# Performance work log

Measured on AMD Instinct MI355X. Metric: run time of the kernel, lower is better.

## Reference

```python
import jax, jax.numpy as jnp
import numpy as np

EPS = 1e-7
MAX_TANGENT_NORM = 1.5
SCALE = 16.0 / 8.0  # alpha / rank


def _exp_map_zero(vs, K, max_norm):
    # vs: [..., n] spatial tangent at origin (time component is 0).
    # Returns (x0, xs): Lorentz point time/spatial parts, <x,x>_L = -1/K.
    sqrtK = jnp.sqrt(K)
    n = jnp.linalg.norm(vs, axis=-1, keepdims=True)
    nc = jnp.minimum(n, max_norm)                       # clamp tangent norm (TB-PAG)
    vs_c = vs * (nc / jnp.maximum(n, EPS))
    t = sqrtK * nc
    x0 = jnp.cosh(t) / sqrtK
    xs = jnp.sinh(t) / (sqrtK * jnp.maximum(nc, EPS)) * vs_c
    return x0, xs


def _log_map_zero_spatial(x0, xs, K):
    # Inverse of exp at origin; returns spatial part of tangent vector.
    sqrtK = jnp.sqrt(K)
    d = jnp.arccosh(jnp.maximum(sqrtK * x0, 1.0 + EPS)) / sqrtK  # geodesic distance
    ns = jnp.linalg.norm(xs, axis=-1, keepdims=True)
    return d * xs / jnp.maximum(ns, EPS)


def setup_inputs() -> dict:
    key = jax.random.key(0)
    k1, k2, k3, k4, k5 = jax.random.split(key, 5)
    Bsz, S, D, R = 4, 2048, 4096, 8
    x = jax.random.normal(k1, (Bsz, S, D), dtype=jnp.float32)
    W = jax.random.normal(k2, (D, D), dtype=jnp.float32) * (1.0 / np.sqrt(D))
    b = jax.random.normal(k3, (D,), dtype=jnp.float32) * 0.01
    A = jax.random.normal(k4, (D, R), dtype=jnp.float32) * 0.01
    B = jax.random.normal(k5, (R, D), dtype=jnp.float32) * 0.01
    log_K = jnp.zeros((), dtype=jnp.float32)  # K = 1.0
    return {"x": x, "W": W, "b": b, "A": A, "B": B, "log_K": log_K}


def reference(x, W, b, A, B, log_K):
    K = jnp.clip(jnp.exp(log_K), 1e-4, 10.0)
    # frozen Euclidean base: z = x @ W^T + b
    z_base = jnp.einsum('bsd,od->bso', x, W) + b
    # project Euclidean hidden state onto H^n: exp_map_zero([0, x])
    x0, xs = _exp_map_zero(x, K, MAX_TANGENT_NORM)
    # LLR: tangent vector at origin, rank-r bottleneck, back to manifold
    v = _log_map_zero_spatial(x0, xs, K)            # [b,s,d]
    v_adapted = (v @ A) @ B                          # rank-8 bottleneck
    y0, ys = _exp_map_zero(v_adapted, K, MAX_TANGENT_NORM)
    # project back to Euclidean (spatial slice of log map)
    delta = _log_map_zero_spatial(y0, ys, K)
    return z_base + delta * SCALE
```

## Files before the change

### kernel.cpp

```cpp
#include <hip/hip_runtime.h>
#include <hip/hip_bf16.h>


#define DD 4096
#define MR 8192
#define BM 256
#define BN 256
#define BK 64

typedef float f32x4 __attribute__((ext_vector_type(4)));
typedef __bf16 bf16x8 __attribute__((ext_vector_type(8)));

#define GLOAD_LDS16(gptr, lptr)                                                        \
  __builtin_amdgcn_global_load_lds((const __attribute__((address_space(1))) void*)(gptr), \
                                   (__attribute__((address_space(3))) void*)(lptr), 16, 0, 0)

__device__ __forceinline__ __bf16 f2bf(float f) { return (__bf16)f; }

__global__ __launch_bounds__(256) void k_prep(const float* __restrict__ x,
                                              const float* __restrict__ W,
                                              const float* __restrict__ A,
                                              const float* __restrict__ Bm,
                                              __bf16* __restrict__ Xb,
                                              __bf16* __restrict__ Wb,
                                              float* __restrict__ U,
                                              float* __restrict__ G) {
  int bid = blockIdx.x;
  int t = threadIdx.x;
  int lane = t & 63, wid = t >> 6;

  if (bid == 0) {
    float g[64];
#pragma unroll
    for (int i = 0; i < 64; ++i) g[i] = 0.f;
    for (int d = t; d < DD; d += 256) {
      float br[8];
#pragma unroll
      for (int r = 0; r < 8; ++r) br[r] = Bm[r * DD + d];
#pragma unroll
      for (int r = 0; r < 8; ++r)
#pragma unroll
        for (int s = 0; s < 8; ++s) g[r * 8 + s] += br[r] * br[s];
    }
    __shared__ float gs[4][64];
#pragma unroll
    for (int i = 0; i < 64; ++i) {
      float v = g[i];
      for (int off = 32; off >= 1; off >>= 1) v += __shfl_down(v, off, 64);
      if (lane == 0) gs[wid][i] = v;
    }
    __syncthreads();
    if (t < 64) G[t] = gs[0][t] + gs[1][t] + gs[2][t] + gs[3][t];
  } else if (bid <= 2048) {
    int r0 = (bid - 1) * 4;
    const float* xr0 = x + (size_t)r0 * DD;
    __bf16* xb0 = Xb + (size_t)r0 * DD;
    float nsq[4] = {0.f, 0.f, 0.f, 0.f};
    float p[4][8] = {};
#pragma unroll
    for (int i = 0; i < 16; ++i) {
      int d = t + 256 * i;
      f32x4 a0 = *reinterpret_cast<const f32x4*>(A + (size_t)d * 8);
      f32x4 a1 = *reinterpret_cast<const f32x4*>(A + (size_t)d * 8 + 4);
#pragma unroll
      for (int r = 0; r < 4; ++r) {
        float xv = xr0[(size_t)r * DD + d];
        xb0[(size_t)r * DD + d] = f2bf(xv);
        nsq[r] += xv * xv;
        p[r][0] += xv * a0[0]; p[r][1] += xv * a0[1];
        p[r][2] += xv * a0[2]; p[r][3] += xv * a0[3];
        p[r][4] += xv * a1[0]; p[r][5] += xv * a1[1];
        p[r][6] += xv * a1[2]; p[r][7] += xv * a1[3];
      }
    }
    for (int off = 32; off >= 1; off >>= 1) {
#pragma unroll
      for (int r = 0; r < 4; ++r) {
        nsq[r] += __shfl_down(nsq[r], off, 64);
#pragma unroll
        for (int q = 0; q < 8; ++q) p[r][q] += __shfl_down(p[r][q], off, 64);
      }
    }
    __shared__ float red[4][36];
    if (lane == 0) {
#pragma unroll
      for (int r = 0; r < 4; ++r) {
        red[wid][r * 9] = nsq[r];
#pragma unroll
        for (int q = 0; q < 8; ++q) red[wid][r * 9 + 1 + q] = p[r][q];
      }
    }
    __syncthreads();
    if (t < 4) {
      float ns = red[0][t * 9] + red[1][t * 9] + red[2][t * 9] + red[3][t * 9];
      float u[8];
#pragma unroll
      for (int q = 0; q < 8; ++q)
        u[q] = red[0][t * 9 + 1 + q] + red[1][t * 9 + 1 + q] +
               red[2][t * 9 + 1 + q] + red[3][t * 9 + 1 + q];
      float n = sqrtf(ns);
      float s1 = fminf(n, 1.5f) / fmaxf(n, 1e-7f);
#pragma unroll
      for (int q = 0; q < 8; ++q) U[(size_t)(r0 + t) * 8 + q] = s1 * u[q];
    }
  } else {
    int i = (bid - 2049) * 256 + t;
    const f32x4* s = reinterpret_cast<const f32x4*>(W) + (size_t)i * 2;
    f32x4 v0 = s[0], v1 = s[1];
    bf16x8 o;
    o[0] = f2bf(v0[0]); o[1] = f2bf(v0[1]); o[2] = f2bf(v0[2]); o[3] = f2bf(v0[3]);
    o[4] = f2bf(v1[0]); o[5] = f2bf(v1[1]); o[6] = f2bf(v1[2]); o[7] = f2bf(v1[3]);
    reinterpret_cast<bf16x8*>(Wb)[i] = o;
  }
}

__global__ __launch_bounds__(512, 2) void k_gemm(const __bf16* __restrict__ Xb,
                                                 const __bf16* __restrict__ Wb,
                                                 const float* __restrict__ bias,
                                                 const float* __restrict__ U,
                                                 const float* __restrict__ G,
                                                 const float* __restrict__ Bm,
                                                 float* __restrict__ out) {
  __shared__ union {
    char raw[131072];
    struct { float cs[256][8]; float bs2[8][256]; } epi;
  } sm;
  char* smc = sm.raw;

  const int nwg = (MR / BM) * (DD / BN);
  int wg = ((int)blockIdx.x % 8) * (nwg / 8) + (int)blockIdx.x / 8;
  int tm = wg / (DD / BN);
  int tn = wg % (DD / BN);
  int row0 = tm * BM, col0 = tn * BN;

  int t = threadIdx.x;
  int lane = t & 63, wid = t >> 6;
  int wm = wid >> 2, wn = wid & 3;
  int fr = lane & 15;
  int hi = lane >> 4;
  int sw = (fr >> 1) & 3;

  f32x4 acc[8][4] = {};
  bf16x8 aF[4], bF[4];

  auto STAGE = [&](const __bf16* mat, int rowbase, int tau, int ks, int ldsOff) {
    int j = (t & 3) ^ ((t >> 3) & 3);
    int kk = ((tau & 63) << 6) + (ks << 5) + (j << 3);
    const __bf16* src = mat + (size_t)(rowbase + (t >> 2)) * DD + kk;
    char* dst = smc + ldsOff + t * 16;
    GLOAD_LDS16(src, dst);
    GLOAD_LDS16(src + (size_t)128 * DD, dst + 8192);
  };

#define LDA(buf, ks, mbase)                                                     \
  _Pragma("unroll") for (int j = 0; j < 4; ++j) aF[j] =                         \
      *reinterpret_cast<const bf16x8*>(smc + (buf)*65536 + 16384 + (ks)*32768 + \
                                       (wm * 128 + ((mbase) + j) * 16 + fr) * 64 + \
                                       ((hi ^ sw) << 4));
#define LDB(buf, ks)                                                            \
  _Pragma("unroll") for (int j = 0; j < 4; ++j) bF[j] =                         \
      *reinterpret_cast<const bf16x8*>(smc + (buf)*65536 + (ks)*32768 +         \
                                       (wn * 64 + j * 16 + fr) * 64 +           \
                                       ((hi ^ sw) << 4));
#define MMQ(mbase)                                                              \
  __builtin_amdgcn_s_setprio(1);                                                \
  _Pragma("unroll") for (int j = 0; j < 4; ++j)                                 \
      _Pragma("unroll") for (int n = 0; n < 4; ++n)                             \
          acc[(mbase) + j][n] = __builtin_amdgcn_mfma_f32_16x16x32_bf16(        \
              aF[j], bF[n], acc[(mbase) + j][n], 0, 0, 0);                      \
  __builtin_amdgcn_s_setprio(0);
#define BAR() __builtin_amdgcn_s_barrier()
#define VM6() asm volatile("s_waitcnt vmcnt(6)" ::: "memory")

  STAGE(Wb, col0, 0, 0, 0);
  STAGE(Xb, row0, 0, 0, 16384);
  STAGE(Wb, col0, 0, 1, 32768);
  STAGE(Xb, row0, 0, 1, 49152);
  asm volatile("s_waitcnt vmcnt(4)" ::: "memory");
  STAGE(Wb, col0, 1, 0, 65536 + 0);
  STAGE(Xb, row0, 1, 0, 65536 + 16384);
  STAGE(Wb, col0, 1, 1, 65536 + 32768);
  VM6();
  BAR();

  for (int i = 0; i < 32; ++i) {
    int T = 2 * i;
    LDA(0, 0, 0); LDB(0, 0);
    STAGE(Xb, row0, T + 1, 1, 65536 + 49152);
    BAR();
    MMQ(0);
    BAR();
    LDA(0, 0, 4);
    STAGE(Wb, col0, T + 2, 0, 0);
    BAR();
    MMQ(4);
    BAR();
    LDA(0, 1, 0); LDB(0, 1);
    STAGE(Xb, row0, T + 2, 0, 16384);
    BAR();
    MMQ(0);
    BAR();
    LDA(0, 1, 4);
    STAGE(Wb, col0, T + 2, 1, 32768);
    BAR();
    MMQ(4);
    VM6();
    BAR();
    LDA(1, 0, 0); LDB(1, 0);
    STAGE(Xb, row0, T + 2, 1, 49152);
    BAR();
    MMQ(0);
    BAR();
    LDA(1, 0, 4);
    STAGE(Wb, col0, T + 3, 0, 65536 + 0);
    BAR();
    MMQ(4);
    BAR();
    LDA(1, 1, 0); LDB(1, 1);
    STAGE(Xb, row0, T + 3, 0, 65536 + 16384);
    BAR();
    MMQ(0);
    BAR();
    LDA(1, 1, 4);
    STAGE(Wb, col0, T + 3, 1, 65536 + 32768);
    BAR();
    MMQ(4);
    VM6();
    BAR();
  }

  asm volatile("s_waitcnt vmcnt(0)" ::: "memory");
  __syncthreads();
  {
    int rr = t >> 6, cc = (t & 63) * 4;
    *reinterpret_cast<f32x4*>(&sm.epi.bs2[rr][cc]) =
        *reinterpret_cast<const f32x4*>(Bm + (size_t)rr * DD + col0 + cc);
  }
  if (t < 256) {
    f32x4 u0 = *reinterpret_cast<const f32x4*>(U + (size_t)(row0 + t) * 8);
    f32x4 u1 = *reinterpret_cast<const f32x4*>(U + (size_t)(row0 + t) * 8 + 4);
    float u[8] = {u0[0], u0[1], u0[2], u0[3], u1[0], u1[1], u1[2], u1[3]};
    float n2sq = 0.f;
#pragma unroll
    for (int r = 0; r < 8; ++r) {
      float s = 0.f;
#pragma unroll
      for (int q = 0; q < 8; ++q) s += G[r * 8 + q] * u[q];
      n2sq += u[r] * s;
    }
    float n2 = sqrtf(fmaxf(n2sq, 0.f));
    float sc2 = 2.0f * fminf(n2, 1.5f) / fmaxf(n2, 1e-7f);
#pragma unroll
    for (int r = 0; r < 8; ++r) sm.epi.cs[t][r] = sc2 * u[r];
  }
  __syncthreads();

  int colb = col0 + wn * 64 + fr;
  float biasv[4], bcol[4][8];
#pragma unroll
  for (int n = 0; n < 4; ++n) {
    biasv[n] = bias[colb + n * 16];
#pragma unroll
    for (int r = 0; r < 8; ++r) bcol[n][r] = sm.epi.bs2[r][wn * 64 + fr + n * 16];
  }
#pragma unroll
  for (int m = 0; m < 8; ++m) {
#pragma unroll
    for (int j = 0; j < 4; ++j) {
      int rl = wm * 128 + m * 16 + hi * 4 + j;
      float c0 = sm.epi.cs[rl][0], c1 = sm.epi.cs[rl][1], c2 = sm.epi.cs[rl][2],
            c3 = sm.epi.cs[rl][3], c4 = sm.epi.cs[rl][4], c5 = sm.epi.cs[rl][5],
            c6 = sm.epi.cs[rl][6], c7 = sm.epi.cs[rl][7];
      float* orow = out + (size_t)(row0 + rl) * DD + colb;
#pragma unroll
      for (int n = 0; n < 4; ++n) {
        float delta = c0 * bcol[n][0] + c1 * bcol[n][1] + c2 * bcol[n][2] +
                      c3 * bcol[n][3] + c4 * bcol[n][4] + c5 * bcol[n][5] +
                      c6 * bcol[n][6] + c7 * bcol[n][7];
        orow[n * 16] = acc[m][n][j] + biasv[n] + delta;
      }
    }
  }
}

extern "C" void kernel_launch(void* const* d_in, const int* in_sizes, int n_in,
                              void* d_out, int out_size, void* d_ws, size_t ws_size,
                              hipStream_t stream) {
  const float* x = (const float*)d_in[0];
  const float* W = (const float*)d_in[1];
  const float* b = (const float*)d_in[2];
  const float* A = (const float*)d_in[3];
  const float* Bm = (const float*)d_in[4];
  float* out = (float*)d_out;

  char* ws = (char*)d_ws;
  __bf16* Xb = (__bf16*)ws;
  __bf16* Wb = (__bf16*)(ws + (size_t)64 * 1024 * 1024);
  float* U = (float*)(ws + (size_t)96 * 1024 * 1024);
  float* G = (float*)(ws + (size_t)96 * 1024 * 1024 + 256 * 1024);

  k_prep<<<1 + 2048 + 8192, 256, 0, stream>>>(x, W, A, Bm, Xb, Wb, U, G);
  k_gemm<<<(MR / BM) * (DD / BN), 512, 0, stream>>>(Xb, Wb, b, U, G, Bm, out);
}
```

Measured before the change: 306.9 us.

## Restructure GEMM main loop into whole-tile compute then batched staging

Replaces the fine-grained interleaving of LDS reads, MFMA groups and per-quarter global-to-LDS stages (each fenced by barriers) with a coarser schedule. Each loop step now computes a whole K-tile from one buffer, then issues all four stage loads for the next tile into that buffer, with the vmcnt threshold raised to match. This removes about 16 barriers per iteration, cutting synchronisation overhead, at the cost of bursty memory issue and less overlap between loads and MFMAs within a tile. It also stages the fourth quarter in the prologue instead of inside the loop.

```diff
diff --git a/kernel.cpp b/kernel.cpp
--- a/kernel.cpp
+++ b/kernel.cpp
@@ -170,62 +170,46 @@
               aF[j], bF[n], acc[(mbase) + j][n], 0, 0, 0);                      \
   __builtin_amdgcn_s_setprio(0);
 #define BAR() __builtin_amdgcn_s_barrier()
-#define VM6() asm volatile("s_waitcnt vmcnt(6)" ::: "memory")
+#define VM8() asm volatile("s_waitcnt vmcnt(8)" ::: "memory")
+
+#define KTILE(buf)                                                              \
+  LDA(buf, 0, 0); LDB(buf, 0);                                                  \
+  MMQ(0);                                                                       \
+  LDA(buf, 0, 4);                                                               \
+  MMQ(4);                                                                       \
+  LDA(buf, 1, 0); LDB(buf, 1);                                                  \
+  MMQ(0);                                                                       \
+  LDA(buf, 1, 4);                                                               \
+  MMQ(4)
 
   STAGE(Wb, col0, 0, 0, 0);
   STAGE(Xb, row0, 0, 0, 16384);
   STAGE(Wb, col0, 0, 1, 32768);
   STAGE(Xb, row0, 0, 1, 49152);
-  asm volatile("s_waitcnt vmcnt(4)" ::: "memory");
   STAGE(Wb, col0, 1, 0, 65536 + 0);
   STAGE(Xb, row0, 1, 0, 65536 + 16384);
   STAGE(Wb, col0, 1, 1, 65536 + 32768);
-  VM6();
+  STAGE(Xb, row0, 1, 1, 65536 + 49152);
+  VM8();
   BAR();
 
   for (int i = 0; i < 32; ++i) {
     int T = 2 * i;
-    LDA(0, 0, 0); LDB(0, 0);
-    STAGE(Xb, row0, T + 1, 1, 65536 + 49152);
-    BAR();
-    MMQ(0);
-    BAR();
-    LDA(0, 0, 4);
+    KTILE(0);
+    BAR();
     STAGE(Wb, col0, T + 2, 0, 0);
-    BAR();
-    MMQ(4);
-    BAR();
-    LDA(0, 1, 0); LDB(0, 1);
     STAGE(Xb, row0, T + 2, 0, 16384);
-    BAR();
-    MMQ(0);
-    BAR();
-    LDA(0, 1, 4);
     STAGE(Wb, col0, T + 2, 1, 32768);
-    BAR();
-    MMQ(4);
-    VM6();
-    BAR();
-    LDA(1, 0, 0); LDB(1, 0);
     STAGE(Xb, row0, T + 2, 1, 49152);
-    BAR();
-    MMQ(0);
-    BAR();
-    LDA(1, 0, 4);
+    VM8();
+    BAR();
+    KTILE(1);
+    BAR();
     STAGE(Wb, col0, T + 3, 0, 65536 + 0);
-    BAR();
-    MMQ(4);
-    BAR();
-    LDA(1, 1, 0); LDB(1, 1);
     STAGE(Xb, row0, T + 3, 0, 65536 + 16384);
-    BAR();
-    MMQ(0);
-    BAR();
-    LDA(1, 1, 4);
     STAGE(Wb, col0, T + 3, 1, 65536 + 32768);
-    BAR();
-    MMQ(4);
-    VM6();
+    STAGE(Xb, row0, T + 3, 1, 65536 + 49152);
+    VM8();
     BAR();
   }
 
```

After: 355.8 us. 15.9% more time.
